# Performance work log

Hardware: AMD Instinct MI355X
Metric: run time of the kernel (lower is better)

## Reference

```python
import jax, jax.numpy as jnp
import numpy as np

VOCAB, D_MODEL, N_HEADS, D_FF = 32000, 2048, 16, 8192
B, S = 2, 2048
HEAD_DIM = D_MODEL // N_HEADS
EPS = 1e-6


def setup_inputs() -> dict:
    key = jax.random.key(0)
    ks = jax.random.split(key, 12)
    sc = 0.02
    return {
        "tokens": jax.random.randint(ks[0], (B, S), 0, VOCAB),
        "tok_emb": jax.random.normal(ks[1], (VOCAB, D_MODEL), jnp.float32) * sc,
        "wq": jax.random.normal(ks[2], (D_MODEL, D_MODEL), jnp.float32) * sc,
        "wk": jax.random.normal(ks[3], (D_MODEL, D_MODEL), jnp.float32) * sc,
        "wv": jax.random.normal(ks[4], (D_MODEL, D_MODEL), jnp.float32) * sc,
        "wo": jax.random.normal(ks[5], (D_MODEL, D_MODEL), jnp.float32) * sc,
        "attn_norm_w": jnp.ones((D_MODEL,), jnp.float32),
        "ffn_norm_w": jnp.ones((D_MODEL,), jnp.float32),
        "final_norm_w": jnp.ones((D_MODEL,), jnp.float32),
        "w1": jax.random.normal(ks[6], (D_FF, D_MODEL), jnp.float32) * sc,
        "w2": jax.random.normal(ks[7], (D_MODEL, D_FF), jnp.float32) * sc,
        "out_proj": jax.random.normal(ks[8], (VOCAB, D_MODEL), jnp.float32) * sc,
    }


def rms_norm(x, w):
    return w * x * jax.lax.rsqrt(jnp.mean(x * x, axis=-1, keepdims=True) + EPS)


def reference(tokens, tok_emb, wq, wk, wv, wo, attn_norm_w, ffn_norm_w,
              final_norm_w, w1, w2, out_proj):
    x = tok_emb[tokens]  # [B, S, D]
    b, s, _ = x.shape

    # --- attention (explicit causal QK^T + softmax, as in source) ---
    xn = rms_norm(x, attn_norm_w)
    q = (xn @ wq.T).reshape(b, s, N_HEADS, HEAD_DIM)
    k = (xn @ wk.T).reshape(b, s, N_HEADS, HEAD_DIM)
    v = (xn @ wv.T).reshape(b, s, N_HEADS, HEAD_DIM)
    scores = jnp.einsum("bqhd,bkhd->bhqk", q, k) * (HEAD_DIM ** -0.5)
    causal = jnp.triu(jnp.ones((s, s), dtype=bool), k=1)  # True above diag
    scores = jnp.where(causal, -jnp.inf, scores)
    attn = jax.nn.softmax(scores, axis=-1)
    out = jnp.einsum("bhqk,bkhd->bqhd", attn, v).reshape(b, s, -1)
    x = x + out @ wo.T

    # --- FFN (world_size=1: all_gather/reduce_scatter are identities) ---
    hn = rms_norm(x, ffn_norm_w)
    h = jax.nn.silu(hn @ w1.T) @ w2.T
    x = x + h

    logits = rms_norm(x, final_norm_w) @ out_proj.T  # [B, S, VOCAB]
    return logits
```

## Files before the change

### kernel.cpp

```cpp
#include <hip/hip_runtime.h>
#include <stdint.h>

#define DM     2048
#define NHE    16
#define DFF    8192
#define NBATCH 2
#define SEQ    2048
#define NTOK   4096
#define HD     128
#define NVOCAB 32000

typedef __attribute__((ext_vector_type(8))) short short8;
typedef __attribute__((ext_vector_type(4))) float f32x4;
typedef __attribute__((ext_vector_type(4))) unsigned short u16x4;

static __device__ __forceinline__ unsigned short f2b(float f) {
  union { float f; uint32_t u; } v; v.f = f;
  return (unsigned short)((v.u + 0x7FFFu + ((v.u >> 16) & 1u)) >> 16);
}

static __device__ __forceinline__ void gload16(const void* g, void* l) {
  __builtin_amdgcn_global_load_lds(
      (const __attribute__((address_space(1))) unsigned int*)g,
      (__attribute__((address_space(3))) unsigned int*)l, 16, 0, 0);
}

__global__ void k_f32_to_bf16(const float* __restrict__ in,
                              unsigned short* __restrict__ out, int nq) {
  int i = blockIdx.x * blockDim.x + threadIdx.x;
  int stride = gridDim.x * blockDim.x;
  for (; i < nq; i += stride) {
    float4 v = ((const float4*)in)[i];
    u16x4 o;
    o.x = f2b(v.x); o.y = f2b(v.y); o.z = f2b(v.z); o.w = f2b(v.w);
    ((u16x4*)out)[i] = o;
  }
}

__global__ void k_embed(const int* __restrict__ tok,
                        const float* __restrict__ emb, float* __restrict__ x) {
  int n = blockIdx.x;
  int t = tok[n];
  const float4* src = (const float4*)(emb + (size_t)t * DM);
  float4* dst = (float4*)(x + (size_t)n * DM);
  for (int i = threadIdx.x; i < DM / 4; i += blockDim.x) dst[i] = src[i];
}

__global__ void k_rmsnorm(const float* __restrict__ x, const float* __restrict__ wt,
                          unsigned short* __restrict__ out) {
  int n = blockIdx.x;
  const float* row = x + (size_t)n * DM;
  float ss = 0.f;
  #pragma unroll
  for (int it = 0; it < 2; ++it) {
    int i = threadIdx.x * 4 + it * 1024;
    float4 v = *(const float4*)(row + i);
    ss += v.x * v.x + v.y * v.y + v.z * v.z + v.w * v.w;
  }
  #pragma unroll
  for (int m = 1; m < 64; m <<= 1) ss += __shfl_xor(ss, m);
  __shared__ float p[4];
  if ((threadIdx.x & 63) == 0) p[threadIdx.x >> 6] = ss;
  __syncthreads();
  float inv = rsqrtf((p[0] + p[1] + p[2] + p[3]) * (1.f / DM) + 1e-6f);
  #pragma unroll
  for (int it = 0; it < 2; ++it) {
    int i = threadIdx.x * 4 + it * 1024;
    float4 v = *(const float4*)(row + i);
    float4 w4 = *(const float4*)(wt + i);
    u16x4 o;
    o.x = f2b(v.x * w4.x * inv); o.y = f2b(v.y * w4.y * inv);
    o.z = f2b(v.z * w4.z * inv); o.w = f2b(v.w * w4.w * inv);
    *(u16x4*)(out + (size_t)n * DM + i) = o;
  }
}

#define EPI_BF16  0
#define EPI_RESID 1
#define EPI_SILU  2
#define EPI_F32   3

template <int EPI>
__launch_bounds__(512, 2)
__global__ void k_gemm_nt(const unsigned short* __restrict__ A,
                          const unsigned short* __restrict__ Bm,
                          int M, int N, int K,
                          float* __restrict__ Cf, unsigned short* __restrict__ Cb,
                          const float* __restrict__ R) {
  __shared__ unsigned short lds[2][32768];
  int nbn = N >> 8;
  int nwg = gridDim.x;
  int bid = blockIdx.x;
  int cpx = nwg >> 3;
  bid = (bid & 7) * cpx + (bid >> 3);
  int bm = bid / nbn, bn = bid % nbn;
  int t = threadIdx.x, w = t >> 6, lane = t & 63;
  int wr = w >> 2, wc = w & 3;
  int g = lane >> 4, l15 = lane & 15;

  f32x4 acc[8][4] = {};

  size_t abase = (size_t)(bm * 256) * K;
  size_t bbase = (size_t)(bn * 256) * K;
  int nkt = K >> 6;

  auto stage = [&](int buf, int kt) {
    unsigned short* dst = lds[buf];
    int k0 = kt << 6;
    #pragma unroll
    for (int i = 0; i < 4; ++i) {
      int pos = (i * 512 + t) << 4;
      int row = pos >> 7, colb = pos & 127;
      int csrc = colb ^ ((row & 7) << 4);
      gload16(A + abase + (size_t)row * K + k0 + (csrc >> 1), (char*)dst + pos);
    }
    #pragma unroll
    for (int i = 0; i < 4; ++i) {
      int pos = (i * 512 + t) << 4;
      int row = pos >> 7, colb = pos & 127;
      int csrc = colb ^ ((row & 7) << 4);
      gload16(Bm + bbase + (size_t)row * K + k0 + (csrc >> 1),
              (char*)(dst + 16384) + pos);
    }
  };

  stage(0, 0);
  for (int kt = 0; kt < nkt; ++kt) {
    int cur = kt & 1;
    if (kt + 1 < nkt) {
      stage(1 - cur, kt + 1);
      asm volatile("s_waitcnt vmcnt(8)" ::: "memory");
    } else {
      asm volatile("s_waitcnt vmcnt(0)" ::: "memory");
    }
    __builtin_amdgcn_s_barrier();
    __builtin_amdgcn_sched_barrier(0);

    const unsigned short* abuf = lds[cur];
    const unsigned short* bbuf = abuf + 16384;
    __builtin_amdgcn_s_setprio(1);
    #pragma unroll
    for (int kk = 0; kk < 2; ++kk) {
      short8 af[8], bfr[4];
      #pragma unroll
      for (int mm = 0; mm < 8; ++mm) {
        int row = wr * 128 + mm * 16 + l15;
        int col = kk * 64 + g * 16;
        af[mm] = *(const short8*)((const char*)abuf + row * 128 + (col ^ ((row & 7) << 4)));
      }
      #pragma unroll
      for (int nn = 0; nn < 4; ++nn) {
        int row = wc * 64 + nn * 16 + l15;
        int col = kk * 64 + g * 16;
        bfr[nn] = *(const short8*)((const char*)bbuf + row * 128 + (col ^ ((row & 7) << 4)));
      }
      #pragma unroll
      for (int mm = 0; mm < 8; ++mm)
        #pragma unroll
        for (int nn = 0; nn < 4; ++nn)
          acc[mm][nn] = __builtin_amdgcn_mfma_f32_16x16x32_bf16(af[mm], bfr[nn], acc[mm][nn], 0, 0, 0);
    }
    __builtin_amdgcn_s_setprio(0);
    __builtin_amdgcn_sched_barrier(0);
    __builtin_amdgcn_s_barrier();
  }

  #pragma unroll
  for (int mm = 0; mm < 8; ++mm) {
    #pragma unroll
    for (int nn = 0; nn < 4; ++nn) {
      #pragma unroll
      for (int r = 0; r < 4; ++r) {
        int grow = bm * 256 + wr * 128 + mm * 16 + g * 4 + r;
        int gcol = bn * 256 + wc * 64 + nn * 16 + l15;
        size_t off = (size_t)grow * N + gcol;
        float v = acc[mm][nn][r];
        if (EPI == EPI_BF16) {
          Cb[off] = f2b(v);
        } else if (EPI == EPI_RESID) {
          Cf[off] = R[off] + v;
        } else if (EPI == EPI_SILU) {
          float s = 1.f / (1.f + __expf(-v));
          Cb[off] = f2b(v * s);
        } else {
          Cf[off] = v;
        }
      }
    }
  }
}

__global__ void k_transpose_v(const unsigned short* __restrict__ v, int vstride,
                              unsigned short* __restrict__ vt) {
  __shared__ unsigned short tile[64][136];
  int pr = blockIdx.x >> 5;
  int st = blockIdx.x & 31;
  int bb = pr >> 4, h = pr & 15;
  int row = threadIdx.x >> 2;
  int cq = threadIdx.x & 3;
  const unsigned short* src =
      v + (size_t)(bb * SEQ + st * 64 + row) * vstride + h * HD + cq * 32;
  #pragma unroll
  for (int j = 0; j < 4; ++j)
    *(short8*)&tile[row][cq * 32 + j * 8] = *(const short8*)(src + j * 8);
  __syncthreads();
  int d = threadIdx.x >> 1;
  int sh = threadIdx.x & 1;
  unsigned short tmp[32];
  #pragma unroll
  for (int j = 0; j < 32; ++j) tmp[j] = tile[sh * 32 + j][d];
  unsigned short* dst = vt + ((size_t)pr * HD + d) * SEQ + st * 64 + sh * 32;
  #pragma unroll
  for (int j = 0; j < 4; ++j)
    *(short8*)(dst + j * 8) = *(const short8*)&tmp[j * 8];
}

__launch_bounds__(256)
__global__ void k_attn(const unsigned short* __restrict__ q,
                       const unsigned short* __restrict__ k,
                       const unsigned short* __restrict__ vt,
                       unsigned short* __restrict__ ao, int qk_stride) {
  __shared__ unsigned short k_lds[64 * 128];
  __shared__ unsigned short vt_lds[128 * 64];
  __shared__ unsigned short p_lds[4][32 * 64];

  int bid = blockIdx.x;
  int pr = bid >> 4;
  int qt = 15 - (bid & 15);
  int bb = pr >> 4, h = pr & 15;
  int t = threadIdx.x, w = t >> 6, lane = t & 63;
  int g = lane >> 4, l15 = lane & 15;
  const float SCL = 0.08838834764831845f * 1.4426950408889634f;

  int qrow_base = qt * 128 + w * 32;
  short8 aq[2][4];
  #pragma unroll
  for (int mm = 0; mm < 2; ++mm) {
    size_t n = (size_t)(bb * SEQ + qrow_base + mm * 16 + l15);
    #pragma unroll
    for (int kk = 0; kk < 4; ++kk)
      aq[mm][kk] = *(const short8*)(q + n * qk_stride + h * HD + kk * 32 + g * 8);
  }

  f32x4 o[2][8] = {};
  float m2[2][4], ls[2][4];
  #pragma unroll
  for (int mm = 0; mm < 2; ++mm)
    #pragma unroll
    for (int r = 0; r < 4; ++r) { m2[mm][r] = -1e30f; ls[mm][r] = 0.f; }

  int nkv = 2 * qt + 2;
  for (int kvt = 0; kvt < nkv; ++kvt) {
    #pragma unroll
    for (int i = 0; i < 4; ++i) {
      int pos = ((i * 4 + w) << 10) + lane * 16;
      {
        int row = pos >> 8, csw = pos & 255;
        int csrc = csw ^ ((row & 7) << 4);
        gload16(k + (size_t)(bb * SEQ + kvt * 64 + row) * qk_stride + h * HD + (csrc >> 1),
                (char*)k_lds + ((i * 4 + w) << 10));
      }
      {
        int row = pos >> 7, csw = pos & 127;
        int csrc = csw ^ ((row & 7) << 4);
        gload16(vt + ((size_t)pr * HD + row) * SEQ + kvt * 64 + (csrc >> 1),
                (char*)vt_lds + ((i * 4 + w) << 10));
      }
    }
    __syncthreads();

    f32x4 s[2][4] = {};
    #pragma unroll
    for (int kk = 0; kk < 4; ++kk) {
      short8 bk[4];
      #pragma unroll
      for (int nn = 0; nn < 4; ++nn) {
        int row = nn * 16 + l15;
        int col = kk * 64 + g * 16;
        bk[nn] = *(const short8*)((const char*)k_lds + row * 256 + (col ^ ((row & 7) << 4)));
      }
      #pragma unroll
      for (int mm = 0; mm < 2; ++mm)
        #pragma unroll
        for (int nn = 0; nn < 4; ++nn)
          s[mm][nn] = __builtin_amdgcn_mfma_f32_16x16x32_bf16(aq[mm][kk], bk[nn], s[mm][nn], 0, 0, 0);
    }

    bool diag = (kvt >= 2 * qt);
    #pragma unroll
    for (int mm = 0; mm < 2; ++mm) {
      float mx[4] = {-1e30f, -1e30f, -1e30f, -1e30f};
      #pragma unroll
      for (int nn = 0; nn < 4; ++nn)
        #pragma unroll
        for (int r = 0; r < 4; ++r) {
          float sv = s[mm][nn][r] * SCL;
          if (diag) {
            int kvg = kvt * 64 + nn * 16 + l15;
            int qg = qrow_base + mm * 16 + g * 4 + r;
            if (kvg > qg) sv = -1e30f;
          }
          s[mm][nn][r] = sv;
          mx[r] = fmaxf(mx[r], sv);
        }
      #pragma unroll
      for (int r = 0; r < 4; ++r) {
        mx[r] = fmaxf(mx[r], __shfl_xor(mx[r], 1));
        mx[r] = fmaxf(mx[r], __shfl_xor(mx[r], 2));
        mx[r] = fmaxf(mx[r], __shfl_xor(mx[r], 4));
        mx[r] = fmaxf(mx[r], __shfl_xor(mx[r], 8));
        float mn = fmaxf(m2[mm][r], mx[r]);
        float al = exp2f(m2[mm][r] - mn);
        m2[mm][r] = mn;
        ls[mm][r] *= al;
        #pragma unroll
        for (int dd = 0; dd < 8; ++dd) o[mm][dd][r] *= al;
      }
      #pragma unroll
      for (int nn = 0; nn < 4; ++nn)
        #pragma unroll
        for (int r = 0; r < 4; ++r) {
          float pv = exp2f(s[mm][nn][r] - m2[mm][r]);
          ls[mm][r] += pv;
          int row = mm * 16 + g * 4 + r;
          int colb = (nn * 16 + l15) * 2;
          *(unsigned short*)((char*)p_lds[w] + row * 128 + (colb ^ (((row >> 1) & 7) << 4))) = f2b(pv);
        }
    }

    #pragma unroll
    for (int kk = 0; kk < 2; ++kk) {
      short8 pf[2], vf[8];
      #pragma unroll
      for (int mm = 0; mm < 2; ++mm) {
        int row = mm * 16 + l15;
        int col = kk * 64 + g * 16;
        pf[mm] = *(const short8*)((const char*)p_lds[w] + row * 128 + (col ^ (((row >> 1) & 7) << 4)));
      }
      #pragma unroll
      for (int dd = 0; dd < 8; ++dd) {
        int row = dd * 16 + l15;
        int col = kk * 64 + g * 16;
        vf[dd] = *(const short8*)((const char*)vt_lds + row * 128 + (col ^ ((row & 7) << 4)));
      }
      #pragma unroll
      for (int mm = 0; mm < 2; ++mm)
        #pragma unroll
        for (int dd = 0; dd < 8; ++dd)
          o[mm][dd] = __builtin_amdgcn_mfma_f32_16x16x32_bf16(pf[mm], vf[dd], o[mm][dd], 0, 0, 0);
    }
    __syncthreads();
  }

  #pragma unroll
  for (int mm = 0; mm < 2; ++mm) {
    float inv[4];
    #pragma unroll
    for (int r = 0; r < 4; ++r) {
      float tt = ls[mm][r];
      tt += __shfl_xor(tt, 1);
      tt += __shfl_xor(tt, 2);
      tt += __shfl_xor(tt, 4);
      tt += __shfl_xor(tt, 8);
      inv[r] = 1.f / tt;
    }
    #pragma unroll
    for (int dd = 0; dd < 8; ++dd)
      #pragma unroll
      for (int r = 0; r < 4; ++r) {
        size_t n = (size_t)(bb * SEQ + qrow_base + mm * 16 + g * 4 + r);
        int col = h * HD + dd * 16 + l15;
        ao[n * DM + col] = f2b(o[mm][dd][r] * inv[r]);
      }
  }
}

extern "C" void kernel_launch(void* const* d_in, const int* in_sizes, int n_in,
                              void* d_out, int out_size, void* d_ws, size_t ws_size,
                              hipStream_t stream) {
  const int* tokens = (const int*)d_in[0];
  const float* tok_emb = (const float*)d_in[1];
  const float* wq = (const float*)d_in[2];
  const float* wk = (const float*)d_in[3];
  const float* wv = (const float*)d_in[4];
  const float* wo = (const float*)d_in[5];
  const float* attn_nw = (const float*)d_in[6];
  const float* ffn_nw = (const float*)d_in[7];
  const float* final_nw = (const float*)d_in[8];
  const float* w1 = (const float*)d_in[9];
  const float* w2 = (const float*)d_in[10];
  const float* out_proj = (const float*)d_in[11];
  float* out = (float*)d_out;

  char* ws = (char*)d_ws;
  size_t off = 0;
  auto alloc = [&](size_t bytes) -> char* {
    char* p = ws + off;
    off += (bytes + 255) & ~(size_t)255;
    return p;
  };
  unsigned short* wqkv_b = (unsigned short*)alloc((size_t)3 * DM * DM * 2);
  unsigned short* wo_b = (unsigned short*)alloc((size_t)DM * DM * 2);
  unsigned short* w1_b = (unsigned short*)alloc((size_t)DFF * DM * 2);
  unsigned short* w2_b = (unsigned short*)alloc((size_t)DM * DFF * 2);
  unsigned short* wop_b = (unsigned short*)alloc((size_t)NVOCAB * DM * 2);
  float* x = (float*)alloc((size_t)NTOK * DM * 4);
  unsigned short* xn = (unsigned short*)alloc((size_t)NTOK * DM * 2);
  unsigned short* qkv_b = (unsigned short*)alloc((size_t)NTOK * 3 * DM * 2);
  unsigned short* vt_b = (unsigned short*)alloc((size_t)NTOK * DM * 2);
  unsigned short* ao_b = (unsigned short*)alloc((size_t)NTOK * DM * 2);
  unsigned short* h1_b = qkv_b;

  auto conv = [&](const float* src, unsigned short* dst, size_t n) {
    int nq = (int)(n / 4);
    int grid = (nq + 255) / 256;
    if (grid > 4096) grid = 4096;
    k_f32_to_bf16<<<grid, 256, 0, stream>>>(src, dst, nq);
  };
  conv(wq, wqkv_b, (size_t)DM * DM);
  conv(wk, wqkv_b + (size_t)DM * DM, (size_t)DM * DM);
  conv(wv, wqkv_b + (size_t)2 * DM * DM, (size_t)DM * DM);
  conv(wo, wo_b, (size_t)DM * DM);
  conv(w1, w1_b, (size_t)DFF * DM);
  conv(w2, w2_b, (size_t)DM * DFF);
  conv(out_proj, wop_b, (size_t)NVOCAB * DM);

  k_embed<<<NTOK, 256, 0, stream>>>(tokens, tok_emb, x);
  k_rmsnorm<<<NTOK, 256, 0, stream>>>(x, attn_nw, xn);

  k_gemm_nt<EPI_BF16><<<(NTOK / 256) * (3 * DM / 256), 512, 0, stream>>>(
      xn, wqkv_b, NTOK, 3 * DM, DM, nullptr, qkv_b, nullptr);

  k_transpose_v<<<32 * 32, 256, 0, stream>>>(qkv_b + 2 * DM, 3 * DM, vt_b);
  k_attn<<<32 * 16, 256, 0, stream>>>(qkv_b, qkv_b + DM, vt_b, ao_b, 3 * DM);

  k_gemm_nt<EPI_RESID><<<(NTOK / 256) * (DM / 256), 512, 0, stream>>>(
      ao_b, wo_b, NTOK, DM, DM, x, nullptr, x);

  k_rmsnorm<<<NTOK, 256, 0, stream>>>(x, ffn_nw, xn);
  k_gemm_nt<EPI_SILU><<<(NTOK / 256) * (DFF / 256), 512, 0, stream>>>(
      xn, w1_b, NTOK, DFF, DM, nullptr, h1_b, nullptr);
  k_gemm_nt<EPI_RESID><<<(NTOK / 256) * (DM / 256), 512, 0, stream>>>(
      h1_b, w2_b, NTOK, DM, DFF, x, nullptr, x);

  k_rmsnorm<<<NTOK, 256, 0, stream>>>(x, final_nw, xn);
  k_gemm_nt<EPI_F32><<<(NTOK / 256) * (NVOCAB / 256), 512, 0, stream>>>(
      xn, wop_b, NTOK, NVOCAB, DM, out, nullptr, nullptr);
}
```

Before: 1.458 ms.

## Templatize GEMM tile height, add grouped block mapping and sub-tile MFMA interleave

The GEMM kernel takes a row-tile template parameter, and the two DM-wide residual GEMMs use 128-row tiles, doubling their workgroup count on the 256-CU-class device. A grouped block-index mapping (GN column tiles per group) is added for L2 reuse, and the vocab GEMM groups 25 column tiles. The inner loop now loads B fragments once, then processes A in four quarter-chunks with barriers and lgkmcnt waits between them, so LDS reads interleave with MFMA. The extra barriers per k-step may add synchronization overhead.

```diff
diff --git a/kernel.cpp b/kernel.cpp
--- a/kernel.cpp
+++ b/kernel.cpp
@@ -80,35 +80,44 @@
 #define EPI_SILU  2
 #define EPI_F32   3
 
-template <int EPI>
+template <int EPI, int TM>
 __launch_bounds__(512, 2)
 __global__ void k_gemm_nt(const unsigned short* __restrict__ A,
                           const unsigned short* __restrict__ Bm,
-                          int M, int N, int K,
+                          int M, int N, int K, int GN,
                           float* __restrict__ Cf, unsigned short* __restrict__ Cb,
                           const float* __restrict__ R) {
-  __shared__ unsigned short lds[2][32768];
+  constexpr int ALDS = TM * 64;
+  constexpr int MM = TM / 32;
+  constexpr int MQ = MM / 4;
+  __shared__ unsigned short lds[2 * (ALDS + 16384)];
+
+  int nbm = M / TM;
   int nbn = N >> 8;
   int nwg = gridDim.x;
   int bid = blockIdx.x;
   int cpx = nwg >> 3;
   bid = (bid & 7) * cpx + (bid >> 3);
-  int bm = bid / nbn, bn = bid % nbn;
+  int grpsz = nbm * GN;
+  int gg = bid / grpsz, rr = bid % grpsz;
+  int bm = rr / GN;
+  int bn = gg * GN + rr % GN;
+  (void)nbn;
   int t = threadIdx.x, w = t >> 6, lane = t & 63;
   int wr = w >> 2, wc = w & 3;
   int g = lane >> 4, l15 = lane & 15;
 
-  f32x4 acc[8][4] = {};
-
-  size_t abase = (size_t)(bm * 256) * K;
+  f32x4 acc[MM][4] = {};
+
+  size_t abase = (size_t)(bm * TM) * K;
   size_t bbase = (size_t)(bn * 256) * K;
   int nkt = K >> 6;
 
   auto stage = [&](int buf, int kt) {
-    unsigned short* dst = lds[buf];
+    unsigned short* dst = lds + buf * (ALDS + 16384);
     int k0 = kt << 6;
     #pragma unroll
-    for (int i = 0; i < 4; ++i) {
+    for (int i = 0; i < TM / 64; ++i) {
       int pos = (i * 512 + t) << 4;
       int row = pos >> 7, colb = pos & 127;
       int csrc = colb ^ ((row & 7) << 4);
@@ -120,7 +129,7 @@
       int row = pos >> 7, colb = pos & 127;
       int csrc = colb ^ ((row & 7) << 4);
       gload16(Bm + bbase + (size_t)row * K + k0 + (csrc >> 1),
-              (char*)(dst + 16384) + pos);
+              (char*)(dst + ALDS) + pos);
     }
   };
 
@@ -129,49 +138,67 @@
     int cur = kt & 1;
     if (kt + 1 < nkt) {
       stage(1 - cur, kt + 1);
-      asm volatile("s_waitcnt vmcnt(8)" ::: "memory");
+      if constexpr (TM == 256) {
+        asm volatile("s_waitcnt vmcnt(8)" ::: "memory");
+      } else {
+        asm volatile("s_waitcnt vmcnt(6)" ::: "memory");
+      }
     } else {
       asm volatile("s_waitcnt vmcnt(0)" ::: "memory");
     }
     __builtin_amdgcn_s_barrier();
     __builtin_amdgcn_sched_barrier(0);
 
-    const unsigned short* abuf = lds[cur];
-    const unsigned short* bbuf = abuf + 16384;
-    __builtin_amdgcn_s_setprio(1);
-    #pragma unroll
-    for (int kk = 0; kk < 2; ++kk) {
-      short8 af[8], bfr[4];
-      #pragma unroll
-      for (int mm = 0; mm < 8; ++mm) {
-        int row = wr * 128 + mm * 16 + l15;
-        int col = kk * 64 + g * 16;
-        af[mm] = *(const short8*)((const char*)abuf + row * 128 + (col ^ ((row & 7) << 4)));
-      }
-      #pragma unroll
-      for (int nn = 0; nn < 4; ++nn) {
+    const unsigned short* abuf = lds + cur * (ALDS + 16384);
+    const unsigned short* bbuf = abuf + ALDS;
+
+    short8 bfr[4][2];
+    #pragma unroll
+    for (int nn = 0; nn < 4; ++nn)
+      #pragma unroll
+      for (int kk = 0; kk < 2; ++kk) {
         int row = wc * 64 + nn * 16 + l15;
         int col = kk * 64 + g * 16;
-        bfr[nn] = *(const short8*)((const char*)bbuf + row * 128 + (col ^ ((row & 7) << 4)));
-      }
-      #pragma unroll
-      for (int mm = 0; mm < 8; ++mm)
+        bfr[nn][kk] = *(const short8*)((const char*)bbuf + row * 128 + (col ^ ((row & 7) << 4)));
+      }
+
+    #pragma unroll
+    for (int q = 0; q < 4; ++q) {
+      short8 af[MQ][2];
+      #pragma unroll
+      for (int mi = 0; mi < MQ; ++mi)
+        #pragma unroll
+        for (int kk = 0; kk < 2; ++kk) {
+          int row = wr * (TM / 2) + (q * MQ + mi) * 16 + l15;
+          int col = kk * 64 + g * 16;
+          af[mi][kk] = *(const short8*)((const char*)abuf + row * 128 + (col ^ ((row & 7) << 4)));
+        }
+      __builtin_amdgcn_s_barrier();
+      asm volatile("s_waitcnt lgkmcnt(0)" ::: "memory");
+      __builtin_amdgcn_sched_barrier(0);
+      __builtin_amdgcn_s_setprio(1);
+      #pragma unroll
+      for (int mi = 0; mi < MQ; ++mi)
         #pragma unroll
         for (int nn = 0; nn < 4; ++nn)
-          acc[mm][nn] = __builtin_amdgcn_mfma_f32_16x16x32_bf16(af[mm], bfr[nn], acc[mm][nn], 0, 0, 0);
-    }
-    __builtin_amdgcn_s_setprio(0);
-    __builtin_amdgcn_sched_barrier(0);
-    __builtin_amdgcn_s_barrier();
-  }
-
-  #pragma unroll
-  for (int mm = 0; mm < 8; ++mm) {
+          #pragma unroll
+          for (int kk = 0; kk < 2; ++kk)
+            acc[q * MQ + mi][nn] =
+                __builtin_amdgcn_mfma_f32_16x16x32_bf16(af[mi][kk], bfr[nn][kk],
+                                                        acc[q * MQ + mi][nn], 0, 0, 0);
+      __builtin_amdgcn_s_setprio(0);
+      __builtin_amdgcn_sched_barrier(0);
+      __builtin_amdgcn_s_barrier();
+    }
+  }
+
+  #pragma unroll
+  for (int mm = 0; mm < MM; ++mm) {
     #pragma unroll
     for (int nn = 0; nn < 4; ++nn) {
       #pragma unroll
       for (int r = 0; r < 4; ++r) {
-        int grow = bm * 256 + wr * 128 + mm * 16 + g * 4 + r;
+        int grow = bm * TM + wr * (TM / 2) + mm * 16 + g * 4 + r;
         int gcol = bn * 256 + wc * 64 + nn * 16 + l15;
         size_t off = (size_t)grow * N + gcol;
         float v = acc[mm][nn][r];
@@ -428,22 +455,22 @@
   k_embed<<<NTOK, 256, 0, stream>>>(tokens, tok_emb, x);
   k_rmsnorm<<<NTOK, 256, 0, stream>>>(x, attn_nw, xn);
 
-  k_gemm_nt<EPI_BF16><<<(NTOK / 256) * (3 * DM / 256), 512, 0, stream>>>(
-      xn, wqkv_b, NTOK, 3 * DM, DM, nullptr, qkv_b, nullptr);
+  k_gemm_nt<EPI_BF16, 256><<<(NTOK / 256) * (3 * DM / 256), 512, 0, stream>>>(
+      xn, wqkv_b, NTOK, 3 * DM, DM, 3 * DM / 256, nullptr, qkv_b, nullptr);
 
   k_transpose_v<<<32 * 32, 256, 0, stream>>>(qkv_b + 2 * DM, 3 * DM, vt_b);
   k_attn<<<32 * 16, 256, 0, stream>>>(qkv_b, qkv_b + DM, vt_b, ao_b, 3 * DM);
 
-  k_gemm_nt<EPI_RESID><<<(NTOK / 256) * (DM / 256), 512, 0, stream>>>(
-      ao_b, wo_b, NTOK, DM, DM, x, nullptr, x);
+  k_gemm_nt<EPI_RESID, 128><<<(NTOK / 128) * (DM / 256), 512, 0, stream>>>(
+      ao_b, wo_b, NTOK, DM, DM, DM / 256, x, nullptr, x);
 
   k_rmsnorm<<<NTOK, 256, 0, stream>>>(x, ffn_nw, xn);
-  k_gemm_nt<EPI_SILU><<<(NTOK / 256) * (DFF / 256), 512, 0, stream>>>(
-      xn, w1_b, NTOK, DFF, DM, nullptr, h1_b, nullptr);
-  k_gemm_nt<EPI_RESID><<<(NTOK / 256) * (DM / 256), 512, 0, stream>>>(
-      h1_b, w2_b, NTOK, DM, DFF, x, nullptr, x);
+  k_gemm_nt<EPI_SILU, 256><<<(NTOK / 256) * (DFF / 256), 512, 0, stream>>>(
+      xn, w1_b, NTOK, DFF, DM, DFF / 256, nullptr, h1_b, nullptr);
+  k_gemm_nt<EPI_RESID, 128><<<(NTOK / 128) * (DM / 256), 512, 0, stream>>>(
+      h1_b, w2_b, NTOK, DM, DFF, DM / 256, x, nullptr, x);
 
   k_rmsnorm<<<NTOK, 256, 0, stream>>>(x, final_nw, xn);
-  k_gemm_nt<EPI_F32><<<(NTOK / 256) * (NVOCAB / 256), 512, 0, stream>>>(
-      xn, wop_b, NTOK, NVOCAB, DM, out, nullptr, nullptr);
-}
+  k_gemm_nt<EPI_F32, 256><<<(NTOK / 256) * (NVOCAB / 256), 512, 0, stream>>>(
+      xn, wop_b, NTOK, NVOCAB, DM, 25, out, nullptr, nullptr);
+}
```

Result: faster. 1.420 ms (-2.6%).
